# Performance work log

Measured on AMD Instinct MI355X. Metric: run time of the kernel, lower is better.

The kernel has to match this reference:

```python
import jax, jax.numpy as jnp
import numpy as np

# Sign with straight-through estimator (XNOR-Net style: grad passes where |x| <= 1)
@jax.custom_vjp
def sign_ste(x):
    return jnp.sign(x)

def _sign_fwd(x):
    return jnp.sign(x), x

def _sign_bwd(x, g):
    return (g * (jnp.abs(x) <= 1.0).astype(g.dtype),)

sign_ste.defvjp(_sign_fwd, _sign_bwd)

STRIDE = (1, 1)
PADDING = ((1, 1), (1, 1))

def _conv(x, w):
    # x: [N,C,H,W], w: [O,I,kh,kw]
    return jax.lax.conv_general_dilated(
        x, w, window_strides=STRIDE, padding=PADDING,
        dimension_numbers=("NCHW", "OIHW", "NCHW"))

def setup_inputs() -> dict:
    key = jax.random.key(0)
    k1, k2, k3 = jax.random.split(key, 3)
    x = jax.random.normal(k1, (32, 256, 56, 56), dtype=jnp.float32)
    weight1 = jax.random.normal(k2, (256, 256, 3, 3), dtype=jnp.float32) * 0.05
    weight2 = jax.random.normal(k3, (256, 256, 3, 3), dtype=jnp.float32) * 0.05
    return {"x": x, "weight1": weight1, "weight2": weight2}

def reference(x, weight1, weight2):
    # alpha: per-output-channel mean |w| averaged over both branches -> [O,1,1]
    alpha = ((jnp.mean(jnp.abs(weight1), axis=(1, 2, 3))
              + jnp.mean(jnp.abs(weight2), axis=(1, 2, 3))) / 2.0)[:, None, None]
    x_sign = sign_ste(x)
    out1 = _conv(x_sign, sign_ste(weight1))
    out2 = _conv(x_sign, sign_ste(weight2))
    return (out1 + out2) * alpha  # broadcast over [N,O,H,W]
```

## Files before the change

### kernel.cpp

```cpp
#include <hip/hip_runtime.h>
#include <hip/hip_bf16.h>
#include <stdint.h>

typedef __attribute__((ext_vector_type(4)))  int   i32x4;
typedef __attribute__((ext_vector_type(8)))  int   i32x8;
typedef __attribute__((ext_vector_type(16))) float f32x16;

typedef const void __attribute__((address_space(1)))* gas_ptr;
typedef void __attribute__((address_space(3)))* las_ptr;
#define GLD16(g, l) __builtin_amdgcn_global_load_lds((gas_ptr)(g), (las_ptr)(l), 16, 0, 0)

#define NIMG 32
#define CIN  256
#define HWDIM 56
#define HPAD 58
#define OCH  256
#define SPATIAL (HWDIM*HWDIM)
#define M_TOT (NIMG*SPATIAL)
#define KTOT  2304
#define NSTEP 18
#define ROWB  128
#define WROWB 1152

#define WT4_OFF   13778944ull
#define ALPHA_OFF 14073856ull

#define LDSBUF 16384

__global__ __launch_bounds__(256)
void prep_weights(const float* __restrict__ w1, const float* __restrict__ w2,
                  unsigned char* __restrict__ WT4, float* __restrict__ alpha) {
    const int o = blockIdx.x;
    const int t = threadIdx.x;
    const float* p1 = w1 + o * KTOT;
    const float* p2 = w2 + o * KTOT;
    unsigned char* wo = WT4 + o * WROWB;

    float s1 = 0.f, s2 = 0.f;
    for (int i = t; i < WROWB; i += 256) {
        int k0  = 2 * i;
        int tap = k0 >> 8;
        int c   = k0 & 255;
        float a0 = p1[c * 9 + tap],       b0 = p2[c * 9 + tap];
        float a1 = p1[(c + 1) * 9 + tap], b1 = p2[(c + 1) * 9 + tap];
        s1 += fabsf(a0) + fabsf(a1);
        s2 += fabsf(b0) + fabsf(b1);
        int sg0 = ((a0 > 0.f) - (a0 < 0.f)) + ((b0 > 0.f) - (b0 < 0.f));
        int sg1 = ((a1 > 0.f) - (a1 < 0.f)) + ((b1 > 0.f) - (b1 < 0.f));
        unsigned e0 = (sg0 == 2) ? 0x4u : (sg0 == 1) ? 0x2u : (sg0 == 0) ? 0x0u
                    : (sg0 == -1) ? 0xAu : 0xCu;
        unsigned e1 = (sg1 == 2) ? 0x4u : (sg1 == 1) ? 0x2u : (sg1 == 0) ? 0x0u
                    : (sg1 == -1) ? 0xAu : 0xCu;
        wo[i] = (unsigned char)(e0 | (e1 << 4));
    }
    __shared__ float red[8];
    #pragma unroll
    for (int off = 32; off > 0; off >>= 1) {
        s1 += __shfl_down(s1, off, 64);
        s2 += __shfl_down(s2, off, 64);
    }
    const int lane = t & 63, wv = t >> 6;
    if (lane == 0) { red[wv] = s1; red[4 + wv] = s2; }
    __syncthreads();
    if (t == 0) {
        float t1 = red[0] + red[1] + red[2] + red[3];
        float t2 = red[4] + red[5] + red[6] + red[7];
        alpha[o] = (t1 * (1.f / 2304.f) + t2 * (1.f / 2304.f)) * 0.5f;
    }
}

__global__ __launch_bounds__(256)
void binarize_kernel(const float* __restrict__ x, unsigned char* __restrict__ xb4) {
    const int b  = blockIdx.x;
    const int n  = b / HPAD;
    const int hp = b % HPAD;
    const int t  = threadIdx.x;
    unsigned char* rowp = xb4 + ((size_t)n * HPAD + hp) * (HPAD * ROWB);

    if (hp == 0 || hp == HPAD - 1) {
        int* ip = (int*)rowp;
        for (int i = t; i < 1856; i += 256) ip[i] = 0;
        return;
    }
    const int h = hp - 1;
    __shared__ __align__(4) unsigned char tile[HWDIM * 132];
    if (t < 224) {
        const int w  = t % HWDIM;
        const int cl = t / HWDIM;
        const float* xp = x + (size_t)n * (CIN * SPATIAL) + (size_t)h * HWDIM + w;
        for (int c0 = cl * 2; c0 < CIN; c0 += 8) {
            float v0 = xp[(size_t)c0 * SPATIAL];
            float v1 = xp[(size_t)(c0 + 1) * SPATIAL];
            unsigned e0 = (v0 > 0.f) ? 0x2u : ((v0 < 0.f) ? 0xAu : 0x0u);
            unsigned e1 = (v1 > 0.f) ? 0x2u : ((v1 < 0.f) ? 0xAu : 0x0u);
            tile[w * 132 + (c0 >> 1)] = (unsigned char)(e0 | (e1 << 4));
        }
    }
    int* ip = (int*)rowp;
    if (t < 32) ip[t] = 0;
    else if (t < 64) ip[57 * 32 + (t - 32)] = 0;
    __syncthreads();
    const int g = t >> 5, lam = t & 31;
    unsigned char* op = rowp + ROWB;
    for (int w0 = 0; w0 < HWDIM; w0 += 8) {
        int w = w0 + g;
        int val = *(const int*)&tile[w * 132 + lam * 4];
        *(int*)(op + (size_t)w * ROWB + lam * 4) = val;
    }
}

__global__ __launch_bounds__(256, 2)
void conv_kernel(const unsigned char* __restrict__ xb4,
                 const unsigned char* __restrict__ WT4,
                 const float* __restrict__ alpha,
                 float* __restrict__ out) {
    __shared__ __align__(16) char lds[4 * LDSBUF];

    const int t    = threadIdx.x;
    const int lane = t & 63;
    const int wv   = t >> 6;

    const int bid  = blockIdx.x;
    const int tid_ = (bid & 7) * 196 + (bid >> 3);
    const int nt   = tid_ & 1;
    const int mt   = tid_ >> 1;
    const int o0   = nt * 128;
    const int m0   = mt * 128;

    const int srow = t >> 1;
    const int sh16 = (t & 1) * 16;
    const unsigned char* w_g = WT4 + (size_t)(o0 + srow) * WROWB + sh16;
    const unsigned char* a_g;
    {
        int m  = m0 + srow;
        int ni = m / SPATIAL;
        int sp = m - ni * SPATIAL;
        int h  = sp / HWDIM;
        int w  = sp - h * HWDIM;
        a_g = xb4 + ((size_t)(ni * HPAD + h) * HPAD + w) * ROWB + sh16;
    }
    char* dstT = lds + t * 16;

    f32x16 acc[2][2];
    #pragma unroll
    for (int i = 0; i < 2; ++i)
        #pragma unroll
        for (int j = 0; j < 2; ++j)
            acc[i][j] = (f32x16){0.f,0.f,0.f,0.f,0.f,0.f,0.f,0.f,
                                 0.f,0.f,0.f,0.f,0.f,0.f,0.f,0.f};

    const int l31 = lane & 31;
    const int l5  = lane >> 5;
    const int wro = ((wv & 1) * 64 + l31) * 32 + l5 * 16;
    const int aro = 8192 + ((wv >> 1) * 64 + l31) * 32 + l5 * 16;

    #define STAGE(S, B)                                                     \
    {                                                                       \
        const int s_ = (S);                                                 \
        const int tap = s_ >> 1;                                            \
        const int kh = tap / 3, kw = tap - kh * 3;                          \
        const int ch = (s_ & 1) * 64;                                       \
        const int aoff = (kh * HPAD + kw) * ROWB + ch;                      \
        const int woff = tap * 128 + ch;                                    \
        char* d = dstT + (B) * LDSBUF;                                      \
        GLD16(w_g + woff,      d);                                          \
        GLD16(w_g + woff + 32, d + 4096);                                   \
        GLD16(a_g + aoff,      d + 8192);                                   \
        GLD16(a_g + aoff + 32, d + 12288);                                  \
    }

    i32x8 wf[2] = {};
    i32x8 xf[2] = {};

    STAGE(0, 0);
    STAGE(1, 1);
    STAGE(2, 2);
    asm volatile("s_waitcnt vmcnt(8)\n\ts_barrier" ::: "memory");

    #pragma unroll
    for (int s = 0; s < NSTEP; ++s) {
        const char* Wb = lds + (s & 3) * LDSBUF;

        if (s + 3 < NSTEP) STAGE(s + 3, (s + 3) & 3);

        #pragma unroll
        for (int ks = 0; ks < 2; ++ks) {
            const char* Kb = Wb + ks * 4096;
            *(i32x4*)&wf[0] = *(const i32x4*)(Kb + wro);
            *(i32x4*)&wf[1] = *(const i32x4*)(Kb + wro + 1024);
            *(i32x4*)&xf[0] = *(const i32x4*)(Kb + aro);
            *(i32x4*)&xf[1] = *(const i32x4*)(Kb + aro + 1024);

            #pragma unroll
            for (int i = 0; i < 2; ++i)
                #pragma unroll
                for (int j = 0; j < 2; ++j)
                    acc[i][j] = __builtin_amdgcn_mfma_scale_f32_32x32x64_f8f6f4(
                        wf[i], xf[j], acc[i][j], 4, 4, 0, 127, 0, 127);
        }

        if (s <= NSTEP - 4)
            asm volatile("s_waitcnt vmcnt(8) lgkmcnt(0)\n\ts_barrier" ::: "memory");
        else if (s == NSTEP - 3)
            asm volatile("s_waitcnt vmcnt(4) lgkmcnt(0)\n\ts_barrier" ::: "memory");
        else if (s == NSTEP - 2)
            asm volatile("s_waitcnt vmcnt(0) lgkmcnt(0)\n\ts_barrier" ::: "memory");
    }

    const int ob0 = o0 + (wv & 1) * 64;
    const int mb0 = m0 + (wv >> 1) * 64;
    #pragma unroll
    for (int j = 0; j < 2; ++j) {
        int m  = mb0 + j * 32 + l31;
        int ni = m / SPATIAL;
        int sp = m - ni * SPATIAL;
        long base = (long)ni * (OCH * SPATIAL) + sp;
        #pragma unroll
        for (int i = 0; i < 2; ++i) {
            #pragma unroll
            for (int r = 0; r < 16; ++r) {
                int o = ob0 + i * 32 + (r & 3) + 8 * (r >> 2) + 4 * l5;
                out[base + (long)o * SPATIAL] = acc[i][j][r] * alpha[o];
            }
        }
    }
    #undef STAGE
}

extern "C" void kernel_launch(void* const* d_in, const int* in_sizes, int n_in,
                              void* d_out, int out_size, void* d_ws, size_t ws_size,
                              hipStream_t stream) {
    const float* x  = (const float*)d_in[0];
    const float* w1 = (const float*)d_in[1];
    const float* w2 = (const float*)d_in[2];
    float* out = (float*)d_out;

    char* ws = (char*)d_ws;
    unsigned char* xb4   = (unsigned char*)ws;
    unsigned char* WT4   = (unsigned char*)(ws + WT4_OFF);
    float*         alpha = (float*)(ws + ALPHA_OFF);

    hipLaunchKernelGGL(prep_weights, dim3(OCH), dim3(256), 0, stream, w1, w2, WT4, alpha);
    hipLaunchKernelGGL(binarize_kernel, dim3(NIMG * HPAD), dim3(256), 0, stream, x, xb4);
    hipLaunchKernelGGL(conv_kernel, dim3((M_TOT / 128) * 2), dim3(256), 0, stream,
                       xb4, WT4, alpha, out);
}
```

Measured before the change: 82.45 us.

## Stage whole taps per step with XOR-swizzled LDS and double buffering

Weights are repacked tap-major so each pipeline step loads a full 128-byte K row (one tap, all channels) for both operands. K steps drop from 18 to 9 and the 4-deep ring of 16KB buffers becomes 2 buffers of 32KB. An XOR swizzle on the 16-byte chunk index is meant to avoid LDS bank conflicts on the fragment reads. The cost is a shallower prefetch (one stage ahead) with a full vmcnt(0) wait per step, which may expose global load latency.

```diff
diff --git a/kernel.cpp b/kernel.cpp
--- a/kernel.cpp
+++ b/kernel.cpp
@@ -18,26 +18,24 @@
 #define SPATIAL (HWDIM*HWDIM)
 #define M_TOT (NIMG*SPATIAL)
 #define KTOT  2304
-#define NSTEP 18
+#define NSTEP 9
 #define ROWB  128
-#define WROWB 1152
 
 #define WT4_OFF   13778944ull
 #define ALPHA_OFF 14073856ull
 
-#define LDSBUF 16384
+#define LDSBUF 32768
 
 __global__ __launch_bounds__(256)
 void prep_weights(const float* __restrict__ w1, const float* __restrict__ w2,
-                  unsigned char* __restrict__ WT4, float* __restrict__ alpha) {
+                  unsigned char* __restrict__ WT4R, float* __restrict__ alpha) {
     const int o = blockIdx.x;
     const int t = threadIdx.x;
     const float* p1 = w1 + o * KTOT;
     const float* p2 = w2 + o * KTOT;
-    unsigned char* wo = WT4 + o * WROWB;
 
     float s1 = 0.f, s2 = 0.f;
-    for (int i = t; i < WROWB; i += 256) {
+    for (int i = t; i < 1152; i += 256) {
         int k0  = 2 * i;
         int tap = k0 >> 8;
         int c   = k0 & 255;
@@ -51,7 +49,8 @@
                     : (sg0 == -1) ? 0xAu : 0xCu;
         unsigned e1 = (sg1 == 2) ? 0x4u : (sg1 == 1) ? 0x2u : (sg1 == 0) ? 0x0u
                     : (sg1 == -1) ? 0xAu : 0xCu;
-        wo[i] = (unsigned char)(e0 | (e1 << 4));
+        WT4R[(size_t)tap * (OCH * ROWB) + o * ROWB + (i & 127)] =
+            (unsigned char)(e0 | (e1 << 4));
     }
     __shared__ float red[8];
     #pragma unroll
@@ -111,10 +110,10 @@
 
 __global__ __launch_bounds__(256, 2)
 void conv_kernel(const unsigned char* __restrict__ xb4,
-                 const unsigned char* __restrict__ WT4,
+                 const unsigned char* __restrict__ WT4R,
                  const float* __restrict__ alpha,
                  float* __restrict__ out) {
-    __shared__ __align__(16) char lds[4 * LDSBUF];
+    __shared__ __align__(16) char lds[2 * LDSBUF];
 
     const int t    = threadIdx.x;
     const int lane = t & 63;
@@ -127,17 +126,19 @@
     const int o0   = nt * 128;
     const int m0   = mt * 128;
 
-    const int srow = t >> 1;
-    const int sh16 = (t & 1) * 16;
-    const unsigned char* w_g = WT4 + (size_t)(o0 + srow) * WROWB + sh16;
-    const unsigned char* a_g;
-    {
-        int m  = m0 + srow;
+    const int sr = t >> 3;
+    const int sx = ((t & 7) ^ (sr & 7)) * 16;
+    const unsigned char* w_g[4];
+    const unsigned char* a_g[4];
+    #pragma unroll
+    for (int q = 0; q < 4; ++q) {
+        w_g[q] = WT4R + (size_t)(o0 + sr + q * 32) * ROWB + sx;
+        int m  = m0 + sr + q * 32;
         int ni = m / SPATIAL;
         int sp = m - ni * SPATIAL;
         int h  = sp / HWDIM;
         int w  = sp - h * HWDIM;
-        a_g = xb4 + ((size_t)(ni * HPAD + h) * HPAD + w) * ROWB + sh16;
+        a_g[q] = xb4 + ((size_t)(ni * HPAD + h) * HPAD + w) * ROWB + sx;
     }
     char* dstT = lds + t * 16;
 
@@ -151,45 +152,45 @@
 
     const int l31 = lane & 31;
     const int l5  = lane >> 5;
-    const int wro = ((wv & 1) * 64 + l31) * 32 + l5 * 16;
-    const int aro = 8192 + ((wv >> 1) * 64 + l31) * 32 + l5 * 16;
+    const int r7  = l31 & 7;
+    const int wr0 = ((wv & 1) * 64 + l31) * ROWB;
+    const int ar0 = 16384 + (((wv >> 1) * 64) + l31) * ROWB;
 
     #define STAGE(S, B)                                                     \
     {                                                                       \
-        const int s_ = (S);                                                 \
-        const int tap = s_ >> 1;                                            \
+        const int tap = (S);                                                \
         const int kh = tap / 3, kw = tap - kh * 3;                          \
-        const int ch = (s_ & 1) * 64;                                       \
-        const int aoff = (kh * HPAD + kw) * ROWB + ch;                      \
-        const int woff = tap * 128 + ch;                                    \
+        const int aoff = (kh * HPAD + kw) * ROWB;                           \
+        const int woff = tap * (OCH * ROWB);                                \
         char* d = dstT + (B) * LDSBUF;                                      \
-        GLD16(w_g + woff,      d);                                          \
-        GLD16(w_g + woff + 32, d + 4096);                                   \
-        GLD16(a_g + aoff,      d + 8192);                                   \
-        GLD16(a_g + aoff + 32, d + 12288);                                  \
-    }
-
-    i32x8 wf[2] = {};
-    i32x8 xf[2] = {};
+        GLD16(w_g[0] + woff, d);                                            \
+        GLD16(w_g[1] + woff, d + 4096);                                     \
+        GLD16(w_g[2] + woff, d + 8192);                                     \
+        GLD16(w_g[3] + woff, d + 12288);                                    \
+        GLD16(a_g[0] + aoff, d + 16384);                                    \
+        GLD16(a_g[1] + aoff, d + 20480);                                    \
+        GLD16(a_g[2] + aoff, d + 24576);                                    \
+        GLD16(a_g[3] + aoff, d + 28672);                                    \
+    }
 
     STAGE(0, 0);
-    STAGE(1, 1);
-    STAGE(2, 2);
-    asm volatile("s_waitcnt vmcnt(8)\n\ts_barrier" ::: "memory");
+    asm volatile("s_waitcnt vmcnt(0)\n\ts_barrier" ::: "memory");
 
     #pragma unroll
     for (int s = 0; s < NSTEP; ++s) {
-        const char* Wb = lds + (s & 3) * LDSBUF;
-
-        if (s + 3 < NSTEP) STAGE(s + 3, (s + 3) & 3);
+        const char* Wb = lds + (s & 1) * LDSBUF;
+
+        if (s + 1 < NSTEP) STAGE(s + 1, (s + 1) & 1);
 
         #pragma unroll
-        for (int ks = 0; ks < 2; ++ks) {
-            const char* Kb = Wb + ks * 4096;
-            *(i32x4*)&wf[0] = *(const i32x4*)(Kb + wro);
-            *(i32x4*)&wf[1] = *(const i32x4*)(Kb + wro + 1024);
-            *(i32x4*)&xf[0] = *(const i32x4*)(Kb + aro);
-            *(i32x4*)&xf[1] = *(const i32x4*)(Kb + aro + 1024);
+        for (int ks = 0; ks < 4; ++ks) {
+            const int off = (((ks << 1) | l5) ^ r7) << 4;
+            i32x8 wf[2] = {};
+            i32x8 xf[2] = {};
+            *(i32x4*)&wf[0] = *(const i32x4*)(Wb + wr0 + off);
+            *(i32x4*)&wf[1] = *(const i32x4*)(Wb + wr0 + 32 * ROWB + off);
+            *(i32x4*)&xf[0] = *(const i32x4*)(Wb + ar0 + off);
+            *(i32x4*)&xf[1] = *(const i32x4*)(Wb + ar0 + 32 * ROWB + off);
 
             #pragma unroll
             for (int i = 0; i < 2; ++i)
@@ -199,11 +200,7 @@
                         wf[i], xf[j], acc[i][j], 4, 4, 0, 127, 0, 127);
         }
 
-        if (s <= NSTEP - 4)
-            asm volatile("s_waitcnt vmcnt(8) lgkmcnt(0)\n\ts_barrier" ::: "memory");
-        else if (s == NSTEP - 3)
-            asm volatile("s_waitcnt vmcnt(4) lgkmcnt(0)\n\ts_barrier" ::: "memory");
-        else if (s == NSTEP - 2)
+        if (s + 1 < NSTEP)
             asm volatile("s_waitcnt vmcnt(0) lgkmcnt(0)\n\ts_barrier" ::: "memory");
     }
 
@@ -237,11 +234,11 @@
 
     char* ws = (char*)d_ws;
     unsigned char* xb4   = (unsigned char*)ws;
-    unsigned char* WT4   = (unsigned char*)(ws + WT4_OFF);
+    unsigned char* WT4R  = (unsigned char*)(ws + WT4_OFF);
     float*         alpha = (float*)(ws + ALPHA_OFF);
 
-    hipLaunchKernelGGL(prep_weights, dim3(OCH), dim3(256), 0, stream, w1, w2, WT4, alpha);
+    hipLaunchKernelGGL(prep_weights, dim3(OCH), dim3(256), 0, stream, w1, w2, WT4R, alpha);
     hipLaunchKernelGGL(binarize_kernel, dim3(NIMG * HPAD), dim3(256), 0, stream, x, xb4);
     hipLaunchKernelGGL(conv_kernel, dim3((M_TOT / 128) * 2), dim3(256), 0, stream,
-                       xb4, WT4, alpha, out);
-}
+                       xb4, WT4R, alpha, out);
+}
```

New measurement: 72.02 us, median of 2. 12.7% less time.
